# Optimization experiments

Measured on AMD Instinct MI355X. Metric: run time of the kernel, lower is better.

## Reference

```python
import jax, jax.numpy as jnp
import numpy as np

BS, N, D = 64, 2048, 512

def setup_inputs() -> dict:
    key = jax.random.key(0)
    ks = jax.random.split(key, 9)
    M = jax.random.uniform(ks[0], (BS, N, D), dtype=jnp.float32)          # memory, uniform(0,1) like M_init
    k = jax.random.normal(ks[1], (BS, D), dtype=jnp.float32)              # key/query
    beta = 5.0 * jax.random.uniform(ks[2], (BS, 1), dtype=jnp.float32)    # content sharpness > 0
    g = jax.random.uniform(ks[3], (BS, 1), dtype=jnp.float32)             # interpolation gate in (0,1)
    s = jax.nn.softmax(jax.random.normal(ks[4], (BS, 3), dtype=jnp.float32), axis=-1)  # shift dist over [-1,0,1]
    y = 1.0 + 2.0 * jax.random.uniform(ks[5], (BS, 1), dtype=jnp.float32) # sharpen exponent >= 1
    e = jax.random.uniform(ks[6], (BS, D), dtype=jnp.float32)             # erase vector in (0,1)
    a = jax.random.normal(ks[7], (BS, D), dtype=jnp.float32)              # add vector
    w_prev = jax.nn.softmax(jax.random.normal(ks[8], (BS, N), dtype=jnp.float32), axis=-1)
    return {"M": M, "k": k, "beta": beta, "g": g, "s": s, "y": y,
            "e": e, "a": a, "w_prev": w_prev}

def reference(M, k, beta, g, s, y, e, a, w_prev):
    # --- content focus: cosine similarity, scaled by beta, softmax over N ---
    dot = jnp.einsum('bnd,bd->bn', M, k)                                   # [bs, N]
    denom = jnp.linalg.norm(M, axis=-1) * jnp.linalg.norm(k, axis=-1, keepdims=True)
    w = jax.nn.softmax((dot / denom) * beta, axis=1)
    # --- location focus: interpolate with previous weights ---
    w = g * w + (1.0 - g) * w_prev
    # --- circular convolution with 3-tap shift kernel s (offsets -1,0,+1) ---
    # original: window [w[i-1], w[i], w[i+1]] dotted with flipped s -> s2*w[i-1]+s1*w[i]+s0*w[i+1]
    w = (s[:, 2:3] * jnp.roll(w, 1, axis=1)
         + s[:, 1:2] * w
         + s[:, 0:1] * jnp.roll(w, -1, axis=1))
    # --- sharpen ---
    wp = w ** y
    w = wp / jnp.sum(wp, axis=1, keepdims=True)                            # [bs, N]
    # --- read ---
    r = jnp.einsum('bn,bnd->bd', w, M)                                     # [bs, D]
    # --- write: M[i] <- M[i] * (1 - w_i * e) + w_i * a  (diag(e) bmm == elementwise) ---
    M_next = M * (1.0 - w[:, :, None] * e[:, None, :]) + w[:, :, None] * a[:, None, :]
    return r, w, M_next
```

## Files before the change

kernel.cpp:

```cpp
#include <hip/hip_runtime.h>

#define BS 64
#define NN 2048
#define DD 512
#define ROWS 64
#define BPB (NN / ROWS)

typedef float f32x4 __attribute__((ext_vector_type(4)));

__global__ __launch_bounds__(256) void k_score(const float* __restrict__ M,
                                               const float* __restrict__ k,
                                               const float* __restrict__ beta,
                                               float* __restrict__ score) {
    int wave = threadIdx.x >> 6;
    int lane = threadIdx.x & 63;
    int row  = blockIdx.x * 4 + wave;
    int b    = row >> 11;
    const float4* Mr = (const float4*)(M + (size_t)row * DD);
    const float4* kr = (const float4*)(k + (size_t)b * DD);
    float dot = 0.f, ssm = 0.f, ssk = 0.f;
#pragma unroll
    for (int i = 0; i < 2; ++i) {
        int idx = lane + i * 64;
        float4 m4 = Mr[idx];
        float4 k4 = kr[idx];
        dot += m4.x * k4.x + m4.y * k4.y + m4.z * k4.z + m4.w * k4.w;
        ssm += m4.x * m4.x + m4.y * m4.y + m4.z * m4.z + m4.w * m4.w;
        ssk += k4.x * k4.x + k4.y * k4.y + k4.z * k4.z + k4.w * k4.w;
    }
#pragma unroll
    for (int off = 32; off > 0; off >>= 1) {
        dot += __shfl_xor(dot, off);
        ssm += __shfl_xor(ssm, off);
        ssk += __shfl_xor(ssk, off);
    }
    if (lane == 0) {
        score[row] = beta[b] * dot * rsqrtf(ssm * ssk);
    }
}

__device__ __forceinline__ float block_max(float v) {
    __shared__ float sm[4];
    int lane = threadIdx.x & 63, wid = threadIdx.x >> 6;
#pragma unroll
    for (int off = 32; off > 0; off >>= 1) v = fmaxf(v, __shfl_xor(v, off));
    if (lane == 0) sm[wid] = v;
    __syncthreads();
    v = fmaxf(fmaxf(sm[0], sm[1]), fmaxf(sm[2], sm[3]));
    __syncthreads();
    return v;
}
__device__ __forceinline__ float block_sum(float v) {
    __shared__ float sm[4];
    int lane = threadIdx.x & 63, wid = threadIdx.x >> 6;
#pragma unroll
    for (int off = 32; off > 0; off >>= 1) v += __shfl_xor(v, off);
    if (lane == 0) sm[wid] = v;
    __syncthreads();
    v = sm[0] + sm[1] + sm[2] + sm[3];
    __syncthreads();
    return v;
}

__global__ __launch_bounds__(256) void k_weights(const float* __restrict__ score,
                                                 const float* __restrict__ gp,
                                                 const float* __restrict__ sp,
                                                 const float* __restrict__ yp,
                                                 const float* __restrict__ w_prev,
                                                 float* __restrict__ w_out) {
    __shared__ float v[NN];
    int b = blockIdx.x, t = threadIdx.x;
    float g  = gp[b], y = yp[b];
    float s0 = sp[b * 3 + 0], s1 = sp[b * 3 + 1], s2 = sp[b * 3 + 2];

    float loc[8];
    float mx = -1e30f;
#pragma unroll
    for (int i = 0; i < 8; ++i) {
        loc[i] = score[b * NN + t * 8 + i];
        mx = fmaxf(mx, loc[i]);
    }
    mx = block_max(mx);
    float sum = 0.f;
#pragma unroll
    for (int i = 0; i < 8; ++i) {
        loc[i] = __expf(loc[i] - mx);
        sum += loc[i];
    }
    sum = block_sum(sum);
    float inv = 1.f / sum;
#pragma unroll
    for (int i = 0; i < 8; ++i) {
        int n = t * 8 + i;
        v[n] = g * loc[i] * inv + (1.f - g) * w_prev[b * NN + n];
    }
    __syncthreads();
    float u[8];
    float psum = 0.f;
#pragma unroll
    for (int i = 0; i < 8; ++i) {
        int n  = t * 8 + i;
        int nm = (n == 0) ? NN - 1 : n - 1;
        int np = (n == NN - 1) ? 0 : n + 1;
        float uu = s2 * v[nm] + s1 * v[n] + s0 * v[np];
        uu = powf(uu, y);
        u[i] = uu;
        psum += uu;
    }
    psum = block_sum(psum);
    float pin = 1.f / psum;
#pragma unroll
    for (int i = 0; i < 8; ++i) w_out[b * NN + t * 8 + i] = u[i] * pin;
}

__global__ __launch_bounds__(256) void k_readwrite(const float* __restrict__ M,
                                                   const float* __restrict__ e,
                                                   const float* __restrict__ a,
                                                   const float* __restrict__ w,
                                                   float* __restrict__ part,
                                                   float* __restrict__ Mn) {
    int blk = (int)gridDim.x - 1 - (int)blockIdx.x;
    int b   = blk / BPB;
    int n0  = (blk % BPB) * ROWS;
    int t   = threadIdx.x;
    int c   = t & 127;
    int rh  = t >> 7;

    const f32x4* e4 = (const f32x4*)(e + (size_t)b * DD);
    const f32x4* a4 = (const f32x4*)(a + (size_t)b * DD);
    f32x4 ev = e4[c], av = a4[c];
    f32x4 acc = (f32x4)(0.f);

    const f32x4* Mb  = (const f32x4*)(M  + ((size_t)b * NN + n0) * DD);
    f32x4*       Mnb = (f32x4*)      (Mn + ((size_t)b * NN + n0) * DD);
    const float* wb  = w + (size_t)b * NN + n0;

    for (int i = 0; i < ROWS / 8; ++i) {
        float  wv[4];
        f32x4  m4[4];
#pragma unroll
        for (int j = 0; j < 4; ++j) {
            int rr = (i * 4 + j) * 2 + rh;
            wv[j] = wb[rr];
            m4[j] = __builtin_nontemporal_load(&Mb[rr * 128 + c]);
        }
#pragma unroll
        for (int j = 0; j < 4; ++j) {
            int rr = (i * 4 + j) * 2 + rh;
            acc += wv[j] * m4[j];
            f32x4 o = m4[j] * (1.f - wv[j] * ev) + wv[j] * av;
            __builtin_nontemporal_store(o, &Mnb[rr * 128 + c]);
        }
    }

    __shared__ f32x4 sacc[128];
    if (rh == 1) sacc[c] = acc;
    __syncthreads();
    if (rh == 0) {
        acc += sacc[c];
        ((f32x4*)(part + (size_t)blk * DD))[c] = acc;
    }
}

__global__ __launch_bounds__(256) void k_reduce(const float* __restrict__ part,
                                               float* __restrict__ r) {
    int b  = blockIdx.x;
    int t  = threadIdx.x;
    int c  = t & 127;
    int rh = t >> 7;
    const f32x4* pb = (const f32x4*)(part + (size_t)b * BPB * DD);
    f32x4 acc = (f32x4)(0.f);
    for (int j = rh * (BPB / 2); j < (rh + 1) * (BPB / 2); ++j) {
        acc += pb[(size_t)j * 128 + c];
    }
    __shared__ f32x4 sacc[128];
    if (rh == 1) sacc[c] = acc;
    __syncthreads();
    if (rh == 0) {
        acc += sacc[c];
        ((f32x4*)(r + (size_t)b * DD))[c] = acc;
    }
}

extern "C" void kernel_launch(void* const* d_in, const int* in_sizes, int n_in,
                              void* d_out, int out_size, void* d_ws, size_t ws_size,
                              hipStream_t stream) {
    const float* M      = (const float*)d_in[0];
    const float* k      = (const float*)d_in[1];
    const float* beta   = (const float*)d_in[2];
    const float* g      = (const float*)d_in[3];
    const float* s      = (const float*)d_in[4];
    const float* y      = (const float*)d_in[5];
    const float* e      = (const float*)d_in[6];
    const float* a      = (const float*)d_in[7];
    const float* w_prev = (const float*)d_in[8];

    float* out = (float*)d_out;
    float* r   = out;
    float* w   = out + BS * DD;
    float* Mn  = out + BS * DD + BS * NN;

    float* score = (float*)d_ws;
    float* part  = score + BS * NN;

    k_score    <<<BS * NN / 4, 256, 0, stream>>>(M, k, beta, score);
    k_weights  <<<BS,          256, 0, stream>>>(score, g, s, y, w_prev, w);
    k_readwrite<<<BS * BPB,    256, 0, stream>>>(M, e, a, w, part, Mn);
    k_reduce   <<<BS,          256, 0, stream>>>(part, r);
}
```

Before: 143.0 us.

## Fuse score, weights and read/write into one kernel with per-batch spin barrier

Merges the scoring, weight computation and read/write kernels into one persistent-style kernel. Eight workgroups per batch each score a 256-row chunk, then synchronize through an atomic flag counter. Each workgroup redundantly computes the full softmax/shift/sharpen for its batch and then streams its chunk of M for the read and write. This removes launch gaps and aims to reuse M from cache between the score pass and the update pass. The cost is a spin barrier across workgroups, which relies on all 512 workgroups being co-resident, plus duplicated weight computation per batch.

```diff
diff --git a/kernel.cpp b/kernel.cpp
--- a/kernel.cpp
+++ b/kernel.cpp
@@ -3,81 +3,115 @@
 #define BS 64
 #define NN 2048
 #define DD 512
-#define ROWS 64
-#define BPB (NN / ROWS)
+#define WGPB 8
+#define CH (NN / WGPB)
+#define NWG (BS * WGPB)
 
 typedef float f32x4 __attribute__((ext_vector_type(4)));
 
-__global__ __launch_bounds__(256) void k_score(const float* __restrict__ M,
-                                               const float* __restrict__ k,
-                                               const float* __restrict__ beta,
-                                               float* __restrict__ score) {
-    int wave = threadIdx.x >> 6;
-    int lane = threadIdx.x & 63;
-    int row  = blockIdx.x * 4 + wave;
-    int b    = row >> 11;
-    const float4* Mr = (const float4*)(M + (size_t)row * DD);
-    const float4* kr = (const float4*)(k + (size_t)b * DD);
-    float dot = 0.f, ssm = 0.f, ssk = 0.f;
-#pragma unroll
-    for (int i = 0; i < 2; ++i) {
-        int idx = lane + i * 64;
-        float4 m4 = Mr[idx];
-        float4 k4 = kr[idx];
-        dot += m4.x * k4.x + m4.y * k4.y + m4.z * k4.z + m4.w * k4.w;
-        ssm += m4.x * m4.x + m4.y * m4.y + m4.z * m4.z + m4.w * m4.w;
-        ssk += k4.x * k4.x + k4.y * k4.y + k4.z * k4.z + k4.w * k4.w;
-    }
-#pragma unroll
-    for (int off = 32; off > 0; off >>= 1) {
-        dot += __shfl_xor(dot, off);
-        ssm += __shfl_xor(ssm, off);
-        ssk += __shfl_xor(ssk, off);
-    }
-    if (lane == 0) {
-        score[row] = beta[b] * dot * rsqrtf(ssm * ssk);
-    }
-}
-
-__device__ __forceinline__ float block_max(float v) {
+__global__ void k_zero(int* __restrict__ flags) {
+    if (threadIdx.x < BS) flags[threadIdx.x] = 0;
+}
+
+__device__ __forceinline__ float block_max(float x) {
     __shared__ float sm[4];
     int lane = threadIdx.x & 63, wid = threadIdx.x >> 6;
 #pragma unroll
-    for (int off = 32; off > 0; off >>= 1) v = fmaxf(v, __shfl_xor(v, off));
-    if (lane == 0) sm[wid] = v;
-    __syncthreads();
-    v = fmaxf(fmaxf(sm[0], sm[1]), fmaxf(sm[2], sm[3]));
-    __syncthreads();
-    return v;
-}
-__device__ __forceinline__ float block_sum(float v) {
+    for (int off = 32; off > 0; off >>= 1) x = fmaxf(x, __shfl_xor(x, off));
+    if (lane == 0) sm[wid] = x;
+    __syncthreads();
+    x = fmaxf(fmaxf(sm[0], sm[1]), fmaxf(sm[2], sm[3]));
+    __syncthreads();
+    return x;
+}
+__device__ __forceinline__ float block_sum(float x) {
     __shared__ float sm[4];
     int lane = threadIdx.x & 63, wid = threadIdx.x >> 6;
 #pragma unroll
-    for (int off = 32; off > 0; off >>= 1) v += __shfl_xor(v, off);
-    if (lane == 0) sm[wid] = v;
-    __syncthreads();
-    v = sm[0] + sm[1] + sm[2] + sm[3];
-    __syncthreads();
-    return v;
-}
-
-__global__ __launch_bounds__(256) void k_weights(const float* __restrict__ score,
-                                                 const float* __restrict__ gp,
-                                                 const float* __restrict__ sp,
-                                                 const float* __restrict__ yp,
-                                                 const float* __restrict__ w_prev,
-                                                 float* __restrict__ w_out) {
+    for (int off = 32; off > 0; off >>= 1) x += __shfl_xor(x, off);
+    if (lane == 0) sm[wid] = x;
+    __syncthreads();
+    x = sm[0] + sm[1] + sm[2] + sm[3];
+    __syncthreads();
+    return x;
+}
+
+__global__ __launch_bounds__(256, 2) void k_fused(
+    const float* __restrict__ M,  const float* __restrict__ kvec,
+    const float* __restrict__ beta, const float* __restrict__ gp,
+    const float* __restrict__ sp, const float* __restrict__ yp,
+    const float* __restrict__ ep, const float* __restrict__ ap,
+    const float* __restrict__ w_prev,
+    float* __restrict__ score, float* __restrict__ part,
+    int* __restrict__ flags,
+    float* __restrict__ w_out, float* __restrict__ Mn)
+{
     __shared__ float v[NN];
-    int b = blockIdx.x, t = threadIdx.x;
-    float g  = gp[b], y = yp[b];
+    __shared__ float wloc[CH];
+    __shared__ f32x4 sacc[128];
+
+    int wg = blockIdx.x;
+    int b  = wg >> 3;
+    int q  = wg & (WGPB - 1);
+    int n0 = q * CH;
+    int t = threadIdx.x, wave = t >> 6, lane = t & 63;
+
+    const f32x4* kr = (const f32x4*)(kvec + (size_t)b * DD);
+    f32x4 k0 = kr[lane], k1 = kr[lane + 64];
+    float ssk = k0.x*k0.x + k0.y*k0.y + k0.z*k0.z + k0.w*k0.w
+              + k1.x*k1.x + k1.y*k1.y + k1.z*k1.z + k1.w*k1.w;
+#pragma unroll
+    for (int off = 32; off > 0; off >>= 1) ssk += __shfl_xor(ssk, off);
+    float bscale = beta[b];
+
+    for (int rloc = wave * 2; rloc < CH; rloc += 8) {
+        int rowA = n0 + rloc, rowB = rowA + 1;
+        const f32x4* MA = (const f32x4*)(M + ((size_t)b * NN + rowA) * DD);
+        const f32x4* MB = (const f32x4*)(M + ((size_t)b * NN + rowB) * DD);
+        f32x4 a0 = MA[lane], a1 = MA[lane + 64];
+        f32x4 b0 = MB[lane], b1 = MB[lane + 64];
+        float dotA = a0.x*k0.x + a0.y*k0.y + a0.z*k0.z + a0.w*k0.w
+                   + a1.x*k1.x + a1.y*k1.y + a1.z*k1.z + a1.w*k1.w;
+        float ssA  = a0.x*a0.x + a0.y*a0.y + a0.z*a0.z + a0.w*a0.w
+                   + a1.x*a1.x + a1.y*a1.y + a1.z*a1.z + a1.w*a1.w;
+        float dotB = b0.x*k0.x + b0.y*k0.y + b0.z*k0.z + b0.w*k0.w
+                   + b1.x*k1.x + b1.y*k1.y + b1.z*k1.z + b1.w*k1.w;
+        float ssB  = b0.x*b0.x + b0.y*b0.y + b0.z*b0.z + b0.w*b0.w
+                   + b1.x*b1.x + b1.y*b1.y + b1.z*b1.z + b1.w*b1.w;
+#pragma unroll
+        for (int off = 32; off > 0; off >>= 1) {
+            dotA += __shfl_xor(dotA, off);
+            ssA  += __shfl_xor(ssA, off);
+            dotB += __shfl_xor(dotB, off);
+            ssB  += __shfl_xor(ssB, off);
+        }
+        if (lane == 0) {
+            score[(size_t)b * NN + rowA] = bscale * dotA * rsqrtf(ssA * ssk);
+            score[(size_t)b * NN + rowB] = bscale * dotB * rsqrtf(ssB * ssk);
+        }
+    }
+
+    __syncthreads();
+    if (t == 0) {
+        __threadfence();
+        __hip_atomic_fetch_add(flags + b, 1, __ATOMIC_RELEASE, __HIP_MEMORY_SCOPE_AGENT);
+        int it = 0;
+        while (__hip_atomic_load(flags + b, __ATOMIC_ACQUIRE, __HIP_MEMORY_SCOPE_AGENT) < WGPB
+               && ++it < (1 << 20)) {
+            __builtin_amdgcn_s_sleep(8);
+        }
+        __threadfence();
+    }
+    __syncthreads();
+
+    float g = gp[b], y = yp[b];
     float s0 = sp[b * 3 + 0], s1 = sp[b * 3 + 1], s2 = sp[b * 3 + 2];
 
     float loc[8];
     float mx = -1e30f;
 #pragma unroll
     for (int i = 0; i < 8; ++i) {
-        loc[i] = score[b * NN + t * 8 + i];
+        loc[i] = score[(size_t)b * NN + t * 8 + i];
         mx = fmaxf(mx, loc[i]);
     }
     mx = block_max(mx);
@@ -92,7 +126,7 @@
 #pragma unroll
     for (int i = 0; i < 8; ++i) {
         int n = t * 8 + i;
-        v[n] = g * loc[i] * inv + (1.f - g) * w_prev[b * NN + n];
+        v[n] = g * loc[i] * inv + (1.f - g) * w_prev[(size_t)b * NN + n];
     }
     __syncthreads();
     float u[8];
@@ -110,55 +144,49 @@
     psum = block_sum(psum);
     float pin = 1.f / psum;
 #pragma unroll
-    for (int i = 0; i < 8; ++i) w_out[b * NN + t * 8 + i] = u[i] * pin;
-}
-
-__global__ __launch_bounds__(256) void k_readwrite(const float* __restrict__ M,
-                                                   const float* __restrict__ e,
-                                                   const float* __restrict__ a,
-                                                   const float* __restrict__ w,
-                                                   float* __restrict__ part,
-                                                   float* __restrict__ Mn) {
-    int blk = (int)gridDim.x - 1 - (int)blockIdx.x;
-    int b   = blk / BPB;
-    int n0  = (blk % BPB) * ROWS;
-    int t   = threadIdx.x;
-    int c   = t & 127;
-    int rh  = t >> 7;
-
-    const f32x4* e4 = (const f32x4*)(e + (size_t)b * DD);
-    const f32x4* a4 = (const f32x4*)(a + (size_t)b * DD);
+    for (int i = 0; i < 8; ++i) {
+        int n = t * 8 + i;
+        if ((n >> 8) == q) {
+            float wf = u[i] * pin;
+            w_out[(size_t)b * NN + n] = wf;
+            wloc[n & (CH - 1)] = wf;
+        }
+    }
+    __syncthreads();
+
+    int c  = t & 127;
+    int rh = t >> 7;
+    const f32x4* e4 = (const f32x4*)(ep + (size_t)b * DD);
+    const f32x4* a4 = (const f32x4*)(ap + (size_t)b * DD);
     f32x4 ev = e4[c], av = a4[c];
     f32x4 acc = (f32x4)(0.f);
 
     const f32x4* Mb  = (const f32x4*)(M  + ((size_t)b * NN + n0) * DD);
     f32x4*       Mnb = (f32x4*)      (Mn + ((size_t)b * NN + n0) * DD);
-    const float* wb  = w + (size_t)b * NN + n0;
-
-    for (int i = 0; i < ROWS / 8; ++i) {
-        float  wv[4];
-        f32x4  m4[4];
-#pragma unroll
-        for (int j = 0; j < 4; ++j) {
-            int rr = (i * 4 + j) * 2 + rh;
-            wv[j] = wb[rr];
-            m4[j] = __builtin_nontemporal_load(&Mb[rr * 128 + c]);
-        }
-#pragma unroll
-        for (int j = 0; j < 4; ++j) {
-            int rr = (i * 4 + j) * 2 + rh;
+
+    for (int i = 0; i < CH / 16; ++i) {
+        float wv[8];
+        f32x4 m4[8];
+#pragma unroll
+        for (int j = 0; j < 8; ++j) {
+            int rr = (i * 8 + j) * 2 + rh;
+            wv[j] = wloc[rr];
+            m4[j] = __builtin_nontemporal_load(&Mb[(size_t)rr * 128 + c]);
+        }
+#pragma unroll
+        for (int j = 0; j < 8; ++j) {
+            int rr = (i * 8 + j) * 2 + rh;
             acc += wv[j] * m4[j];
             f32x4 o = m4[j] * (1.f - wv[j] * ev) + wv[j] * av;
-            __builtin_nontemporal_store(o, &Mnb[rr * 128 + c]);
-        }
-    }
-
-    __shared__ f32x4 sacc[128];
+            __builtin_nontemporal_store(o, &Mnb[(size_t)rr * 128 + c]);
+        }
+    }
+
     if (rh == 1) sacc[c] = acc;
     __syncthreads();
     if (rh == 0) {
         acc += sacc[c];
-        ((f32x4*)(part + (size_t)blk * DD))[c] = acc;
+        ((f32x4*)(part + (size_t)wg * DD))[c] = acc;
     }
 }
 
@@ -168,9 +196,9 @@
     int t  = threadIdx.x;
     int c  = t & 127;
     int rh = t >> 7;
-    const f32x4* pb = (const f32x4*)(part + (size_t)b * BPB * DD);
+    const f32x4* pb = (const f32x4*)(part + (size_t)b * WGPB * DD);
     f32x4 acc = (f32x4)(0.f);
-    for (int j = rh * (BPB / 2); j < (rh + 1) * (BPB / 2); ++j) {
+    for (int j = rh * (WGPB / 2); j < (rh + 1) * (WGPB / 2); ++j) {
         acc += pb[(size_t)j * 128 + c];
     }
     __shared__ f32x4 sacc[128];
@@ -200,11 +228,12 @@
     float* w   = out + BS * DD;
     float* Mn  = out + BS * DD + BS * NN;
 
-    float* score = (float*)d_ws;
-    float* part  = score + BS * NN;
-
-    k_score    <<<BS * NN / 4, 256, 0, stream>>>(M, k, beta, score);
-    k_weights  <<<BS,          256, 0, stream>>>(score, g, s, y, w_prev, w);
-    k_readwrite<<<BS * BPB,    256, 0, stream>>>(M, e, a, w, part, Mn);
-    k_reduce   <<<BS,          256, 0, stream>>>(part, r);
-}
+    int*   flags = (int*)d_ws;
+    float* score = (float*)d_ws + 64;
+    float* part  = score + (size_t)BS * NN;
+
+    k_zero  <<<1,   64, 0, stream>>>(flags);
+    k_fused <<<NWG, 256, 0, stream>>>(M, k, beta, g, s, y, e, a, w_prev,
+                                      score, part, flags, w, Mn);
+    k_reduce<<<BS,  256, 0, stream>>>(part, r);
+}
```

After: 190.2 us. +33.0%, slower.
